# Kernel optimization log

Measured on AMD Instinct MI355X. Metric: run time of the kernel, lower is better.

Reference implementation:

```python
import jax, jax.numpy as jnp
import numpy as np

C = 256
CQK = C // 8  # 32

def setup_inputs() -> dict:
    key = jax.random.key(0)
    ks = jax.random.split(key, 8)
    N, L = 8, 4096
    x = jax.random.normal(ks[0], (N, C, L), dtype=jnp.float32)
    s = 1.0 / np.sqrt(C)
    Wq = jax.random.normal(ks[1], (CQK, C), dtype=jnp.float32) * s
    bq = jnp.zeros((CQK,), dtype=jnp.float32)
    Wk = jax.random.normal(ks[2], (CQK, C), dtype=jnp.float32) * s
    bk = jnp.zeros((CQK,), dtype=jnp.float32)
    Wv = jax.random.normal(ks[3], (C, C), dtype=jnp.float32) * s
    bv = jnp.zeros((C,), dtype=jnp.float32)
    gamma = jnp.ones((1,), dtype=jnp.float32) * 0.5  # nonzero so output depends on attention
    return {"x": x, "Wq": Wq, "bq": bq, "Wk": Wk, "bk": bk, "Wv": Wv, "bv": bv, "gamma": gamma}

def reference(x, Wq, bq, Wk, bk, Wv, bv, gamma):
    # conv1d with kernel_size=1 == pointwise linear over channel dim
    q = jnp.einsum('ncl,oc->nol', x, Wq) + bq[None, :, None]   # (N, C/8, L)
    k = jnp.einsum('ncl,oc->nol', x, Wk) + bk[None, :, None]   # (N, C/8, L)
    v = jnp.einsum('ncl,oc->nol', x, Wv) + bv[None, :, None]   # (N, C, L)
    # energy[n, i, j] = q[n, :, i] . k[n, :, j]
    energy = jnp.einsum('nci,ncj->nij', q, k)                  # (N, L, L)
    attention = jax.nn.softmax(energy, axis=-1)
    # out[n, c, i] = sum_j v[n, c, j] * attention[n, i, j]
    out = jnp.einsum('ncj,nij->nci', v, attention)             # (N, C, L)
    return gamma * out + x
```

## Files before the change

kernel.cpp:

```cpp
#include <hip/hip_runtime.h>
#include <hip/hip_bf16.h>

#define NB 8
#define CC 256
#define LL 4096
#define CQ 32

typedef __bf16 bf16x8 __attribute__((ext_vector_type(8)));
typedef float f32x4 __attribute__((ext_vector_type(4)));
typedef unsigned short u16x4 __attribute__((ext_vector_type(4)));

union B8u { bf16x8 b; u16x4 h[2]; };
union P4u { u16x4 u; __bf16 e[4]; };

#define WS_QT  ((size_t)0)
#define WS_KT  ((size_t)1048576)
#define WS_VV  ((size_t)2097152)
#define WS_WQ  ((size_t)18874368)
#define WS_BQ  ((size_t)18882560)
#define WS_WK  ((size_t)18882592)
#define WS_BK  ((size_t)18890784)
#define WS_WV  ((size_t)18890816)
#define WS_BV  ((size_t)18956352)

__device__ __forceinline__ bool tag_is_bf16(const void* gamma_raw) {
  return *(const unsigned short*)gamma_raw != 0;
}
__device__ __forceinline__ float cvt_load(const void* p, size_t i, bool b16) {
  return b16 ? (float)((const __bf16*)p)[i] : ((const float*)p)[i];
}

__global__ __launch_bounds__(256) void convert_wb_kernel(
    const void* __restrict__ Wq, const void* __restrict__ bq,
    const void* __restrict__ Wk, const void* __restrict__ bk,
    const void* __restrict__ Wv, const void* __restrict__ bv,
    const void* __restrict__ gm, __bf16* __restrict__ ws)
{
  const bool b16 = tag_is_bf16(gm);
  int t = blockIdx.x * 256 + threadIdx.x;
  for (int i = t; i < 82240; i += 32 * 256) {
    float v; size_t dof;
    if (i < 8192)       { v = cvt_load(Wq, i, b16);         dof = WS_WQ + i; }
    else if (i < 8224)  { v = cvt_load(bq, i - 8192, b16);  dof = WS_BQ + (i - 8192); }
    else if (i < 16416) { v = cvt_load(Wk, i - 8224, b16);  dof = WS_WK + (i - 8224); }
    else if (i < 16448) { v = cvt_load(bk, i - 16416, b16); dof = WS_BK + (i - 16416); }
    else if (i < 81984) { v = cvt_load(Wv, i - 16448, b16); dof = WS_WV + (i - 16448); }
    else                { v = cvt_load(bv, i - 81984, b16); dof = WS_BV + (i - 81984); }
    ws[dof] = (__bf16)v;
  }
}

__global__ __launch_bounds__(256, 2) void proj_kernel(
    const void* __restrict__ x_raw, const void* __restrict__ gm_raw,
    __bf16* __restrict__ ws)
{
  const bool b16 = tag_is_bf16(gm_raw);
  const int bid = blockIdx.x;
  const int n = bid & 7, l0 = (bid >> 3) * 64;
  const int tid = threadIdx.x;
  const int w = tid >> 6, lane = tid & 63, li = lane & 15, qd = lane >> 4;

  __shared__ __align__(16) __bf16 tmp[64][72];
  __shared__ __align__(16) __bf16 xlt[64][264];

  for (int cb = 0; cb < 4; ++cb) {
    __syncthreads();
    #pragma unroll
    for (int p = 0; p < 2; ++p) {
      int cc = (tid >> 3) + p * 32;
      int lc = (tid & 7) * 8;
      size_t off = (size_t)n * CC * LL + (size_t)(cb * 64 + cc) * LL + l0 + lc;
      bf16x8 val;
      if (b16) {
        val = *(const bf16x8*)((const __bf16*)x_raw + off);
      } else {
        const float* xf = (const float*)x_raw + off;
        f32x4 a = *(const f32x4*)xf;
        f32x4 b = *(const f32x4*)(xf + 4);
        #pragma unroll
        for (int s = 0; s < 4; ++s) { val[s] = (__bf16)a[s]; val[s + 4] = (__bf16)b[s]; }
      }
      *(bf16x8*)(&tmp[cc][lc]) = val;
    }
    __syncthreads();
    #pragma unroll
    for (int p = 0; p < 2; ++p) {
      int lx = (tid >> 3) + p * 32;
      int cw = (tid & 7) * 8;
      bf16x8 o;
      #pragma unroll
      for (int s = 0; s < 8; ++s) o[s] = tmp[cw + s][lx];
      *(bf16x8*)(&xlt[lx][cb * 64 + cw]) = o;
    }
  }
  __syncthreads();

  const __bf16* Wqk = (w < 2) ? (ws + WS_WQ) : (ws + WS_WK);
  const __bf16* Wv  = ws + WS_WV;
  const int obase = (w & 1) * 16;

  f32x4 vacc[4][4];
  f32x4 qkacc[4];
  #pragma unroll
  for (int a = 0; a < 4; ++a) {
    qkacc[a] = f32x4{0, 0, 0, 0};
    #pragma unroll
    for (int b = 0; b < 4; ++b) vacc[a][b] = f32x4{0, 0, 0, 0};
  }

  for (int k0 = 0; k0 < CC; k0 += 32) {
    bf16x8 xf[4];
    #pragma unroll
    for (int lt = 0; lt < 4; ++lt)
      xf[lt] = *(const bf16x8*)(&xlt[lt * 16 + li][k0 + qd * 8]);
    bf16x8 wa = *(const bf16x8*)(Wqk + (size_t)(obase + li) * CC + k0 + qd * 8);
    #pragma unroll
    for (int lt = 0; lt < 4; ++lt)
      qkacc[lt] = __builtin_amdgcn_mfma_f32_16x16x32_bf16(wa, xf[lt], qkacc[lt], 0, 0, 0);
    #pragma unroll
    for (int ct = 0; ct < 4; ++ct) {
      bf16x8 wb = *(const bf16x8*)(Wv + (size_t)(w * 64 + ct * 16 + li) * CC + k0 + qd * 8);
      #pragma unroll
      for (int lt = 0; lt < 4; ++lt)
        vacc[lt][ct] = __builtin_amdgcn_mfma_f32_16x16x32_bf16(xf[lt], wb, vacc[lt][ct], 0, 0, 0);
    }
  }

  {
    const __bf16* bqk = (w < 2) ? (ws + WS_BQ) : (ws + WS_BK);
    __bf16* dqk = ((w < 2) ? (ws + WS_QT) : (ws + WS_KT)) + (size_t)n * LL * CQ;
    float bf[4];
    #pragma unroll
    for (int rr = 0; rr < 4; ++rr) bf[rr] = (float)bqk[obase + qd * 4 + rr];
    #pragma unroll
    for (int lt = 0; lt < 4; ++lt) {
      P4u pk;
      #pragma unroll
      for (int rr = 0; rr < 4; ++rr) pk.e[rr] = (__bf16)(qkacc[lt][rr] + bf[rr]);
      *(u16x4*)(dqk + (size_t)(l0 + lt * 16 + li) * CQ + obase + qd * 4) = pk.u;
    }
  }
  {
    __bf16* dv = ws + WS_VV + (size_t)n * 128 * CC * 32;
    #pragma unroll
    for (int ct = 0; ct < 4; ++ct) {
      int c = w * 64 + ct * 16 + li;
      float bvf = (float)(ws + WS_BV)[c];
      #pragma unroll
      for (int lt = 0; lt < 4; ++lt) {
        int jl = lt * 16 + qd * 4;
        int jb = (l0 + jl) >> 5, jj = jl & 31;
        P4u pk;
        #pragma unroll
        for (int rr = 0; rr < 4; ++rr) pk.e[rr] = (__bf16)(vacc[lt][ct][rr] + bvf);
        *(u16x4*)(dv + ((size_t)jb * CC + c) * 32 + jj) = pk.u;
      }
    }
  }
}

__global__ __launch_bounds__(512, 4) void attn_kernel(
    const __bf16* __restrict__ ws, const void* __restrict__ x_raw,
    const void* __restrict__ gamma_raw, void* __restrict__ out_raw)
{
  const int bid = blockIdx.x;
  const int n = bid & 7, iblk = (bid >> 3) * 64;
  const int tid = threadIdx.x, w = tid >> 6, lane = tid & 63;
  const int li = lane & 15, qd = lane >> 4;
  const int it = w & 3, jh = w >> 2;
  const int cg = w & 3, jg = w >> 2;

  const __bf16* qtn = ws + WS_QT + (size_t)n * LL * CQ;
  const __bf16* ktn = ws + WS_KT + (size_t)n * LL * CQ;
  const __bf16* v2n = ws + WS_VV + (size_t)n * 128 * CC * 32;

  __shared__ __align__(16) __bf16 plds[2][2][2][4][16][36];
  __shared__ __align__(16) float  lbuf[8][16];
  __shared__ __align__(16) __bf16 olds[256][72];
  float* scratch = (float*)&olds[0][0];

  bf16x8 qfrag = *(const bf16x8*)(qtn + (size_t)(iblk + it * 16 + li) * CQ + qd * 8);
  const f32x4 zero = {0.f, 0.f, 0.f, 0.f};

  f32x4 oacc[16];
  #pragma unroll
  for (int t = 0; t < 16; ++t) oacc[t] = zero;
  float lp = 0.f;

  for (int js = 0; js < LL; js += 128) {
    const int buf = (js >> 7) & 1;
    const int j0 = js + jh * 64;
    const int jv = js + jg * 64;
    bf16x8 kf[4];
    #pragma unroll
    for (int u = 0; u < 4; ++u)
      kf[u] = *(const bf16x8*)(ktn + (size_t)(j0 + u * 16 + li) * CQ + qd * 8);
    bf16x8 vf[4];
    #pragma unroll
    for (int ct = 0; ct < 4; ++ct)
      vf[ct] = *(const bf16x8*)(v2n + ((size_t)(jv >> 5) * CC + cg * 64 + ct * 16 + li) * 32 + qd * 8);
    #pragma unroll
    for (int u = 0; u < 4; ++u) {
      f32x4 s = __builtin_amdgcn_mfma_f32_16x16x32_bf16(kf[u], qfrag, zero, 0, 0, 0);
      P4u pk;
      #pragma unroll
      for (int r = 0; r < 4; ++r) {
        float e = __expf(s[r]); lp += e; pk.e[r] = (__bf16)e;
      }
      *(u16x4*)(&plds[buf][jh][u >> 1][it][li][(u & 1) * 16 + qd * 4]) = pk.u;
    }
    __syncthreads();
    #pragma unroll
    for (int tt = 0; tt < 4; ++tt) {
      B8u ap;
      ap.b = *(const bf16x8*)(&plds[buf][jg][0][tt][li][qd * 8]);
      #pragma unroll
      for (int ct = 0; ct < 4; ++ct)
        oacc[tt * 4 + ct] = __builtin_amdgcn_mfma_f32_16x16x32_bf16(ap.b, vf[ct], oacc[tt * 4 + ct], 0, 0, 0);
    }
    #pragma unroll
    for (int ct = 0; ct < 4; ++ct)
      vf[ct] = *(const bf16x8*)(v2n + ((size_t)((jv + 32) >> 5) * CC + cg * 64 + ct * 16 + li) * 32 + qd * 8);
    #pragma unroll
    for (int tt = 0; tt < 4; ++tt) {
      B8u ap;
      ap.b = *(const bf16x8*)(&plds[buf][jg][1][tt][li][qd * 8]);
      #pragma unroll
      for (int ct = 0; ct < 4; ++ct)
        oacc[tt * 4 + ct] = __builtin_amdgcn_mfma_f32_16x16x32_bf16(ap.b, vf[ct], oacc[tt * 4 + ct], 0, 0, 0);
    }
  }

  lp += __shfl_xor(lp, 16);
  lp += __shfl_xor(lp, 32);
  lbuf[it * 2 + jh][li] = lp;

  #pragma unroll
  for (int r = 0; r < 2; ++r) {
    __syncthreads();
    if (jg == 1 && (cg >> 1) == r) {
      float* d = scratch + (size_t)(cg & 1) * 16 * 256;
      #pragma unroll
      for (int t = 0; t < 16; ++t)
        *(f32x4*)(d + t * 256 + lane * 4) = oacc[t];
    }
    __syncthreads();
    if (jg == 0 && (cg >> 1) == r) {
      const float* s = scratch + (size_t)(cg & 1) * 16 * 256;
      #pragma unroll
      for (int t = 0; t < 16; ++t)
        oacc[t] += *(const f32x4*)(s + t * 256 + lane * 4);
    }
  }
  __syncthreads();

  const bool b16 = tag_is_bf16(gamma_raw);
  const float gma = b16 ? (float)(*(const __bf16*)gamma_raw)
                        : (*(const float*)gamma_raw);

  if (jg == 0) {
    f32x4 gi[4];
    #pragma unroll
    for (int pp = 0; pp < 4; ++pp) {
      f32x4 l0v = *(const f32x4*)(&lbuf[pp * 2 + 0][qd * 4]);
      f32x4 l1v = *(const f32x4*)(&lbuf[pp * 2 + 1][qd * 4]);
      #pragma unroll
      for (int rr = 0; rr < 4; ++rr) gi[pp][rr] = gma / (l0v[rr] + l1v[rr]);
    }
    #pragma unroll
    for (int pp = 0; pp < 4; ++pp) {
      #pragma unroll
      for (int ct = 0; ct < 4; ++ct) {
        P4u pk;
        #pragma unroll
        for (int rr = 0; rr < 4; ++rr)
          pk.e[rr] = (__bf16)(oacc[pp * 4 + ct][rr] * gi[pp][rr]);
        *(u16x4*)(&olds[cg * 64 + ct * 16 + li][pp * 16 + qd * 4]) = pk.u;
      }
    }
  }
  __syncthreads();

  const int i2 = (tid & 31) * 2, c0 = tid >> 5;
  if (b16) {
    const __bf16* xn = (const __bf16*)x_raw + (size_t)n * CC * LL;
    __bf16* outn = (__bf16*)out_raw + (size_t)n * CC * LL;
    for (int c = c0; c < CC; c += 16) {
      unsigned int ov = *(const unsigned int*)(&olds[c][i2]);
      unsigned int xv = *(const unsigned int*)(xn + (size_t)c * LL + iblk + i2);
      const __bf16* op = (const __bf16*)&ov;
      const __bf16* xp = (const __bf16*)&xv;
      unsigned int res;
      __bf16* rp = (__bf16*)&res;
      rp[0] = (__bf16)((float)op[0] + (float)xp[0]);
      rp[1] = (__bf16)((float)op[1] + (float)xp[1]);
      *(unsigned int*)(outn + (size_t)c * LL + iblk + i2) = res;
    }
  } else {
    const float* xn = (const float*)x_raw + (size_t)n * CC * LL;
    float* outn = (float*)out_raw + (size_t)n * CC * LL;
    for (int c = c0; c < CC; c += 16) {
      unsigned int ov = *(const unsigned int*)(&olds[c][i2]);
      const __bf16* op = (const __bf16*)&ov;
      float2 xv = *(const float2*)(xn + (size_t)c * LL + iblk + i2);
      float2 res;
      res.x = (float)op[0] + xv.x;
      res.y = (float)op[1] + xv.y;
      *(float2*)(outn + (size_t)c * LL + iblk + i2) = res;
    }
  }
}

extern "C" void kernel_launch(void* const* d_in, const int* in_sizes, int n_in,
                              void* d_out, int out_size, void* d_ws, size_t ws_size,
                              hipStream_t stream) {
  (void)in_sizes; (void)n_in; (void)out_size; (void)ws_size;
  __bf16* ws = (__bf16*)d_ws;

  hipLaunchKernelGGL(convert_wb_kernel, dim3(32), dim3(256), 0, stream,
                     d_in[1], d_in[2], d_in[3], d_in[4], d_in[5], d_in[6],
                     d_in[7], ws);
  hipLaunchKernelGGL(proj_kernel, dim3(512), dim3(256), 0, stream,
                     d_in[0], d_in[7], ws);
  hipLaunchKernelGGL(attn_kernel, dim3(512), dim3(512), 0, stream,
                     (const __bf16*)ws, d_in[0], d_in[7], d_out);
}
```

Measured before the change: 216.0 us.

## Double attention query tile to 128 rows with 1024-thread blocks and prefetch K

The attention kernel now handles 128 query rows per block with 16 waves instead of 64 rows with 8 waves. Each wave covers 32 output channels instead of 64, so a single V fetch per 128-key step is reused across twice as many query rows. K fragments for the next step are prefetched before the barrier, which removes one mid-loop V reload. The epilogue is split into two 64-row halves to reuse the output LDS buffer. The block count halves to 256, which is about one block per CU and reduces occupancy and latency hiding. The larger block also raises per-thread register and barrier pressure.

Measured after the change: 198.0 us. 1.09x faster.

```diff
diff --git a/kernel.cpp b/kernel.cpp
--- a/kernel.cpp
+++ b/kernel.cpp
@@ -159,25 +159,25 @@
   }
 }
 
-__global__ __launch_bounds__(512, 4) void attn_kernel(
+__global__ __launch_bounds__(1024, 4) void attn_kernel(
     const __bf16* __restrict__ ws, const void* __restrict__ x_raw,
     const void* __restrict__ gamma_raw, void* __restrict__ out_raw)
 {
   const int bid = blockIdx.x;
-  const int n = bid & 7, iblk = (bid >> 3) * 64;
+  const int n = bid & 7, iblk = (bid >> 3) * 128;
   const int tid = threadIdx.x, w = tid >> 6, lane = tid & 63;
   const int li = lane & 15, qd = lane >> 4;
-  const int it = w & 3, jh = w >> 2;
-  const int cg = w & 3, jg = w >> 2;
+  const int it = w & 7, jh = w >> 3;
+  const int cg = w & 7, jg = w >> 3;
 
   const __bf16* qtn = ws + WS_QT + (size_t)n * LL * CQ;
   const __bf16* ktn = ws + WS_KT + (size_t)n * LL * CQ;
   const __bf16* v2n = ws + WS_VV + (size_t)n * 128 * CC * 32;
 
-  __shared__ __align__(16) __bf16 plds[2][2][2][4][16][36];
-  __shared__ __align__(16) float  lbuf[8][16];
+  __shared__ __align__(16) __bf16 plds[2][4][8][16][36];
+  __shared__ __align__(16) float  lbuf[16][16];
   __shared__ __align__(16) __bf16 olds[256][72];
-  float* scratch = (float*)&olds[0][0];
+  float* scratch = (float*)&plds[0][0][0][0][0];
 
   bf16x8 qfrag = *(const bf16x8*)(qtn + (size_t)(iblk + it * 16 + li) * CQ + qd * 8);
   const f32x4 zero = {0.f, 0.f, 0.f, 0.f};
@@ -187,18 +187,21 @@
   for (int t = 0; t < 16; ++t) oacc[t] = zero;
   float lp = 0.f;
 
+  bf16x8 kf[4];
+  #pragma unroll
+  for (int u = 0; u < 4; ++u)
+    kf[u] = *(const bf16x8*)(ktn + (size_t)(jh * 64 + u * 16 + li) * CQ + qd * 8);
+
   for (int js = 0; js < LL; js += 128) {
     const int buf = (js >> 7) & 1;
-    const int j0 = js + jh * 64;
-    const int jv = js + jg * 64;
-    bf16x8 kf[4];
-    #pragma unroll
-    for (int u = 0; u < 4; ++u)
-      kf[u] = *(const bf16x8*)(ktn + (size_t)(j0 + u * 16 + li) * CQ + qd * 8);
     bf16x8 vf[4];
     #pragma unroll
-    for (int ct = 0; ct < 4; ++ct)
-      vf[ct] = *(const bf16x8*)(v2n + ((size_t)(jv >> 5) * CC + cg * 64 + ct * 16 + li) * 32 + qd * 8);
+    for (int s = 0; s < 2; ++s) {
+      const int jb = (js >> 5) + jg * 2 + s;
+      #pragma unroll
+      for (int ct = 0; ct < 2; ++ct)
+        vf[s * 2 + ct] = *(const bf16x8*)(v2n + ((size_t)jb * CC + cg * 32 + ct * 16 + li) * 32 + qd * 8);
+    }
     #pragma unroll
     for (int u = 0; u < 4; ++u) {
       f32x4 s = __builtin_amdgcn_mfma_f32_16x16x32_bf16(kf[u], qfrag, zero, 0, 0, 0);
@@ -207,107 +210,112 @@
       for (int r = 0; r < 4; ++r) {
         float e = __expf(s[r]); lp += e; pk.e[r] = (__bf16)e;
       }
-      *(u16x4*)(&plds[buf][jh][u >> 1][it][li][(u & 1) * 16 + qd * 4]) = pk.u;
-    }
-    __syncthreads();
-    #pragma unroll
-    for (int tt = 0; tt < 4; ++tt) {
-      B8u ap;
-      ap.b = *(const bf16x8*)(&plds[buf][jg][0][tt][li][qd * 8]);
-      #pragma unroll
-      for (int ct = 0; ct < 4; ++ct)
-        oacc[tt * 4 + ct] = __builtin_amdgcn_mfma_f32_16x16x32_bf16(ap.b, vf[ct], oacc[tt * 4 + ct], 0, 0, 0);
-    }
-    #pragma unroll
-    for (int ct = 0; ct < 4; ++ct)
-      vf[ct] = *(const bf16x8*)(v2n + ((size_t)((jv + 32) >> 5) * CC + cg * 64 + ct * 16 + li) * 32 + qd * 8);
-    #pragma unroll
-    for (int tt = 0; tt < 4; ++tt) {
-      B8u ap;
-      ap.b = *(const bf16x8*)(&plds[buf][jg][1][tt][li][qd * 8]);
-      #pragma unroll
-      for (int ct = 0; ct < 4; ++ct)
-        oacc[tt * 4 + ct] = __builtin_amdgcn_mfma_f32_16x16x32_bf16(ap.b, vf[ct], oacc[tt * 4 + ct], 0, 0, 0);
+      *(u16x4*)(&plds[buf][jh * 2 + (u >> 1)][it][li][(u & 1) * 16 + qd * 4]) = pk.u;
+    }
+    {
+      const int jn = (js + 128 < LL) ? (js + 128) : 0;
+      #pragma unroll
+      for (int u = 0; u < 4; ++u)
+        kf[u] = *(const bf16x8*)(ktn + (size_t)(jn + jh * 64 + u * 16 + li) * CQ + qd * 8);
+    }
+    __syncthreads();
+    #pragma unroll
+    for (int s = 0; s < 2; ++s) {
+      #pragma unroll
+      for (int tt = 0; tt < 8; ++tt) {
+        B8u ap;
+        ap.b = *(const bf16x8*)(&plds[buf][jg * 2 + s][tt][li][qd * 8]);
+        oacc[tt * 2 + 0] = __builtin_amdgcn_mfma_f32_16x16x32_bf16(ap.b, vf[s * 2 + 0], oacc[tt * 2 + 0], 0, 0, 0);
+        oacc[tt * 2 + 1] = __builtin_amdgcn_mfma_f32_16x16x32_bf16(ap.b, vf[s * 2 + 1], oacc[tt * 2 + 1], 0, 0, 0);
+      }
     }
   }
 
   lp += __shfl_xor(lp, 16);
   lp += __shfl_xor(lp, 32);
   lbuf[it * 2 + jh][li] = lp;
+  __syncthreads();
 
   #pragma unroll
   for (int r = 0; r < 2; ++r) {
-    __syncthreads();
-    if (jg == 1 && (cg >> 1) == r) {
-      float* d = scratch + (size_t)(cg & 1) * 16 * 256;
+    if (jg == 1 && (cg >> 2) == r) {
+      float* d = scratch + (size_t)(cg & 3) * 4096;
       #pragma unroll
       for (int t = 0; t < 16; ++t)
         *(f32x4*)(d + t * 256 + lane * 4) = oacc[t];
     }
     __syncthreads();
-    if (jg == 0 && (cg >> 1) == r) {
-      const float* s = scratch + (size_t)(cg & 1) * 16 * 256;
+    if (jg == 0 && (cg >> 2) == r) {
+      const float* s = scratch + (size_t)(cg & 3) * 4096;
       #pragma unroll
       for (int t = 0; t < 16; ++t)
         oacc[t] += *(const f32x4*)(s + t * 256 + lane * 4);
     }
-  }
-  __syncthreads();
+    __syncthreads();
+  }
 
   const bool b16 = tag_is_bf16(gamma_raw);
   const float gma = b16 ? (float)(*(const __bf16*)gamma_raw)
                         : (*(const float*)gamma_raw);
 
+  f32x4 gi[8];
   if (jg == 0) {
-    f32x4 gi[4];
-    #pragma unroll
-    for (int pp = 0; pp < 4; ++pp) {
+    #pragma unroll
+    for (int pp = 0; pp < 8; ++pp) {
       f32x4 l0v = *(const f32x4*)(&lbuf[pp * 2 + 0][qd * 4]);
       f32x4 l1v = *(const f32x4*)(&lbuf[pp * 2 + 1][qd * 4]);
       #pragma unroll
       for (int rr = 0; rr < 4; ++rr) gi[pp][rr] = gma / (l0v[rr] + l1v[rr]);
     }
-    #pragma unroll
-    for (int pp = 0; pp < 4; ++pp) {
-      #pragma unroll
-      for (int ct = 0; ct < 4; ++ct) {
-        P4u pk;
+  }
+
+  const int ec = tid >> 5, i2 = (tid & 31) * 2;
+  #pragma unroll
+  for (int h = 0; h < 2; ++h) {
+    if (jg == 0) {
+      #pragma unroll
+      for (int pi = 0; pi < 4; ++pi) {
+        const int pp = h * 4 + pi;
         #pragma unroll
-        for (int rr = 0; rr < 4; ++rr)
-          pk.e[rr] = (__bf16)(oacc[pp * 4 + ct][rr] * gi[pp][rr]);
-        *(u16x4*)(&olds[cg * 64 + ct * 16 + li][pp * 16 + qd * 4]) = pk.u;
-      }
-    }
-  }
-  __syncthreads();
-
-  const int i2 = (tid & 31) * 2, c0 = tid >> 5;
-  if (b16) {
-    const __bf16* xn = (const __bf16*)x_raw + (size_t)n * CC * LL;
-    __bf16* outn = (__bf16*)out_raw + (size_t)n * CC * LL;
-    for (int c = c0; c < CC; c += 16) {
-      unsigned int ov = *(const unsigned int*)(&olds[c][i2]);
-      unsigned int xv = *(const unsigned int*)(xn + (size_t)c * LL + iblk + i2);
-      const __bf16* op = (const __bf16*)&ov;
-      const __bf16* xp = (const __bf16*)&xv;
-      unsigned int res;
-      __bf16* rp = (__bf16*)&res;
-      rp[0] = (__bf16)((float)op[0] + (float)xp[0]);
-      rp[1] = (__bf16)((float)op[1] + (float)xp[1]);
-      *(unsigned int*)(outn + (size_t)c * LL + iblk + i2) = res;
-    }
-  } else {
-    const float* xn = (const float*)x_raw + (size_t)n * CC * LL;
-    float* outn = (float*)out_raw + (size_t)n * CC * LL;
-    for (int c = c0; c < CC; c += 16) {
-      unsigned int ov = *(const unsigned int*)(&olds[c][i2]);
-      const __bf16* op = (const __bf16*)&ov;
-      float2 xv = *(const float2*)(xn + (size_t)c * LL + iblk + i2);
-      float2 res;
-      res.x = (float)op[0] + xv.x;
-      res.y = (float)op[1] + xv.y;
-      *(float2*)(outn + (size_t)c * LL + iblk + i2) = res;
-    }
+        for (int ct = 0; ct < 2; ++ct) {
+          P4u pk;
+          #pragma unroll
+          for (int rr = 0; rr < 4; ++rr)
+            pk.e[rr] = (__bf16)(oacc[pp * 2 + ct][rr] * gi[pp][rr]);
+          *(u16x4*)(&olds[cg * 32 + ct * 16 + li][pi * 16 + qd * 4]) = pk.u;
+        }
+      }
+    }
+    __syncthreads();
+    const int ibase = iblk + h * 64;
+    if (b16) {
+      const __bf16* xn = (const __bf16*)x_raw + (size_t)n * CC * LL;
+      __bf16* outn = (__bf16*)out_raw + (size_t)n * CC * LL;
+      for (int c = ec; c < CC; c += 32) {
+        unsigned int ov = *(const unsigned int*)(&olds[c][i2]);
+        unsigned int xv = *(const unsigned int*)(xn + (size_t)c * LL + ibase + i2);
+        const __bf16* op = (const __bf16*)&ov;
+        const __bf16* xp = (const __bf16*)&xv;
+        unsigned int res;
+        __bf16* rp = (__bf16*)&res;
+        rp[0] = (__bf16)((float)op[0] + (float)xp[0]);
+        rp[1] = (__bf16)((float)op[1] + (float)xp[1]);
+        *(unsigned int*)(outn + (size_t)c * LL + ibase + i2) = res;
+      }
+    } else {
+      const float* xn = (const float*)x_raw + (size_t)n * CC * LL;
+      float* outn = (float*)out_raw + (size_t)n * CC * LL;
+      for (int c = ec; c < CC; c += 32) {
+        unsigned int ov = *(const unsigned int*)(&olds[c][i2]);
+        const __bf16* op = (const __bf16*)&ov;
+        float2 xv = *(const float2*)(xn + (size_t)c * LL + ibase + i2);
+        float2 res;
+        res.x = (float)op[0] + xv.x;
+        res.y = (float)op[1] + xv.y;
+        *(float2*)(outn + (size_t)c * LL + ibase + i2) = res;
+      }
+    }
+    __syncthreads();
   }
 }
 
@@ -322,6 +330,6 @@
                      d_in[7], ws);
   hipLaunchKernelGGL(proj_kernel, dim3(512), dim3(256), 0, stream,
                      d_in[0], d_in[7], ws);
-  hipLaunchKernelGGL(attn_kernel, dim3(512), dim3(512), 0, stream,
+  hipLaunchKernelGGL(attn_kernel, dim3(256), dim3(1024), 0, stream,
                      (const __bf16*)ws, d_in[0], d_in[7], d_out);
 }
```
